# Kernel tuning notes

Hardware: AMD Instinct MI355X
Metric: run time of the kernel (lower is better)

The kernel has to match this reference:

```python
import jax, jax.numpy as jnp
import numpy as np

N = 10000      # nodes
E = 320000     # edges (before self-loops)
D = 256        # d_model
DC = 128       # d_content = d_model // 2
L = 3          # num_layers
K = 4096       # nodes_of_interest
LN_EPS = 1e-5


def setup_inputs() -> dict:
    key = jax.random.key(0)
    ks = jax.random.split(key, 7)
    x = jax.random.normal(ks[0], (N, D), dtype=jnp.float32)
    edge_index = jax.random.randint(ks[1], (2, E), 0, N)
    nodes_of_interest = jax.random.randint(ks[2], (K,), 0, N)
    # per-layer linear weights (stacked over layers)
    Wc = jax.random.normal(ks[3], (L, DC, DC), dtype=jnp.float32) * (1.0 / np.sqrt(DC))
    bc = jnp.zeros((L, DC), dtype=jnp.float32)
    Wp = jax.random.normal(ks[4], (L, DC, DC), dtype=jnp.float32) * (1.0 / np.sqrt(DC))
    bp = jnp.zeros((L, DC), dtype=jnp.float32)
    gamma = jnp.ones((L, D), dtype=jnp.float32)
    beta = jnp.zeros((L, D), dtype=jnp.float32)
    return {"x": x, "edge_index": edge_index, "nodes_of_interest": nodes_of_interest,
            "Wc": Wc, "bc": bc, "Wp": Wp, "bp": bp, "gamma": gamma, "beta": beta}


def _layernorm(h, g, b):
    mu = jnp.mean(h, axis=-1, keepdims=True)
    var = jnp.mean((h - mu) ** 2, axis=-1, keepdims=True)
    return (h - mu) * jax.lax.rsqrt(var + LN_EPS) * g + b


def reference(x, edge_index, nodes_of_interest, Wc, bc, Wp, bp, gamma, beta):
    n = x.shape[0]
    loops = jnp.arange(n)
    # add self-loops (PyG add_self_loops): done per conv in torch but identical each layer
    row = jnp.concatenate([edge_index[0], loops])  # source j
    col = jnp.concatenate([edge_index[1], loops])  # target i
    # symmetric-ish normalization: degree counted over row only (as in source)
    deg = jax.ops.segment_sum(jnp.ones_like(row, dtype=x.dtype), row, num_segments=n)
    dis = deg ** -0.5
    norm = dis[row] * dis[col]  # [E+N]

    def conv(h, l):
        hc = h[:, :DC] @ Wc[l].T + bc[l]
        hp = h[:, DC:] @ Wp[l].T + bp[l]
        ht = jnp.concatenate([hc, hp], axis=-1)
        msg = norm[:, None] * ht[row]                      # gather + normalize
        return jax.ops.segment_sum(msg, col, num_segments=n)  # scatter-add

    for l in range(L - 1):
        x = x + jax.nn.relu(_layernorm(conv(x, l), gamma[l], beta[l]))
    x = x + _layernorm(conv(x, L - 1), gamma[L - 1], beta[L - 1])
    return x[nodes_of_interest]
```

## Files before the change

kernel.cpp:

```cpp
#include <hip/hip_runtime.h>

#define DMODEL 256
#define DCH 128
#define NLAYER 3
#define LN_EPS 1e-5f

__device__ __forceinline__ unsigned short f2bf(float f) {
  unsigned int u = __float_as_uint(f);
  unsigned int r = (u + 0x7FFF + ((u >> 16) & 1)) >> 16;
  return (unsigned short)r;
}


__global__ __launch_bounds__(256) void hist_kernel(const int* __restrict__ row,
    const int* __restrict__ col, int* cnt_row, int* cnt_col, int E) {
  int e = blockIdx.x * 256 + threadIdx.x;
  if (e < E) {
    atomicAdd(&cnt_row[row[e]], 1);
    atomicAdd(&cnt_col[col[e]], 1);
  }
}

__global__ __launch_bounds__(256) void scan_dis_kernel(
    const int* __restrict__ cnt_col, const int* __restrict__ cnt_row,
    int* __restrict__ indptr, int* __restrict__ cursor,
    float* __restrict__ dis, int N, int E) {
  int t = threadIdx.x;
  for (int i = t; i < N; i += 256) dis[i] = rsqrtf((float)(cnt_row[i] + 1));

  const int PER = (N + 255) / 256;
  int start = t * PER;
  int sum = 0;
  for (int k = 0; k < PER; ++k) {
    int i = start + k;
    if (i < N) sum += cnt_col[i];
  }
  int lane = t & 63, wid = t >> 6;
  int inc = sum;
#pragma unroll
  for (int off = 1; off < 64; off <<= 1) {
    int v = __shfl_up(inc, off);
    if (lane >= off) inc += v;
  }
  __shared__ int wsum[4];
  if (lane == 63) wsum[wid] = inc;
  __syncthreads();
  int woff = 0;
  for (int w = 0; w < wid; ++w) woff += wsum[w];
  int run = woff + inc - sum;
  for (int k = 0; k < PER; ++k) {
    int i = start + k;
    if (i < N) {
      indptr[i] = run;
      cursor[i] = run;
      run += cnt_col[i];
    }
  }
  if (t == 255) indptr[N] = E;
}

__global__ __launch_bounds__(256) void fill_kernel(const int* __restrict__ row,
    const int* __restrict__ col, int* cursor, int* __restrict__ idx, int E) {
  int e = blockIdx.x * 256 + threadIdx.x;
  if (e < E) {
    int pos = atomicAdd(&cursor[col[e]], 1);
    idx[pos] = row[e];
  }
}


__global__ __launch_bounds__(256) void gemm_kernel(const float* __restrict__ x,
    const float* __restrict__ Wc, const float* __restrict__ bc,
    const float* __restrict__ Wp, const float* __restrict__ bp,
    unsigned short* __restrict__ ht, int layer, int Nn) {
  int h = blockIdx.y;
  const float* __restrict__ W = (h ? Wp : Wc) + (size_t)layer * DCH * DCH;
  const float* __restrict__ b = (h ? bp : bc) + (size_t)layer * DCH;
  int i0 = blockIdx.x * 32;
  int t = threadIdx.x;
  int tx = t & 31;
  int ty = t >> 5;

  __shared__ float xs[32][128];
  __shared__ float Ws[32][132];

#pragma unroll
  for (int i = 0; i < 4; ++i) {
    int f = t + i * 256;
    int r = f >> 5, cq = f & 31;
    int gi = i0 + r;
    float4 v = make_float4(0.f, 0.f, 0.f, 0.f);
    if (gi < Nn) v = *(const float4*)&x[(size_t)gi * DMODEL + h * DCH + cq * 4];
    *(float4*)&xs[r][cq * 4] = v;
  }

  float acc[4][4];
#pragma unroll
  for (int r = 0; r < 4; ++r)
#pragma unroll
    for (int c = 0; c < 4; ++c) acc[r][c] = 0.f;

  for (int kc = 0; kc < 128; kc += 32) {
    __syncthreads();
#pragma unroll
    for (int i = 0; i < 4; ++i) {
      int f = t + i * 256;
      int o = f >> 3;
      int kq = f & 7;
      float4 v = *(const float4*)&W[o * 128 + kc + kq * 4];
      Ws[kq * 4 + 0][o] = v.x;
      Ws[kq * 4 + 1][o] = v.y;
      Ws[kq * 4 + 2][o] = v.z;
      Ws[kq * 4 + 3][o] = v.w;
    }
    __syncthreads();
#pragma unroll 8
    for (int k = 0; k < 32; ++k) {
      float4 wv = *(const float4*)&Ws[k][tx * 4];
      float xr[4];
#pragma unroll
      for (int r = 0; r < 4; ++r) xr[r] = xs[ty * 4 + r][kc + k];
#pragma unroll
      for (int r = 0; r < 4; ++r) {
        acc[r][0] += xr[r] * wv.x;
        acc[r][1] += xr[r] * wv.y;
        acc[r][2] += xr[r] * wv.z;
        acc[r][3] += xr[r] * wv.w;
      }
    }
  }

  float4 bias = *(const float4*)&b[tx * 4];
#pragma unroll
  for (int r = 0; r < 4; ++r) {
    int gi = i0 + ty * 4 + r;
    if (gi < Nn) {
      ushort4 pk;
      pk.x = f2bf(acc[r][0] + bias.x);
      pk.y = f2bf(acc[r][1] + bias.y);
      pk.z = f2bf(acc[r][2] + bias.z);
      pk.w = f2bf(acc[r][3] + bias.w);
      *(ushort4*)&ht[(size_t)gi * DMODEL + h * DCH + tx * 4] = pk;
    }
  }
}


__global__ __launch_bounds__(128) void agg_kernel(const float* __restrict__ xin,
    const unsigned short* __restrict__ ht, float* __restrict__ xout,
    const float* __restrict__ dis, const int* __restrict__ indptr,
    const int* __restrict__ idx, const float* __restrict__ gamma,
    const float* __restrict__ beta, const int* __restrict__ noi,
    int use_noi, int relu) {
  int b = blockIdx.x;
  int i = use_noi ? noi[b] : b;
  int t = threadIdx.x;
  float di = dis[i];
  size_t rbase = (size_t)i * DMODEL + 2 * t;

  unsigned int us = *(const unsigned int*)&ht[rbase];
  float w2s = di * di;
  float acc0 = w2s * __uint_as_float(us << 16);
  float acc1 = w2s * __uint_as_float(us & 0xFFFF0000u);

  int s = indptr[i], e = indptr[i + 1];
  __shared__ int s_src[128];
  __shared__ float s_w[128];
  for (int base = s; base < e; base += 128) {
    int n = min(128, e - base);
    __syncthreads();
    if (t < n) {
      int sr = idx[base + t];
      s_src[t] = sr;
      s_w[t] = dis[sr] * di;
    }
    __syncthreads();
    for (int j = 0; j < n; ++j) {
      unsigned int u = *(const unsigned int*)&ht[(size_t)s_src[j] * DMODEL + 2 * t];
      float w = s_w[j];
      acc0 += w * __uint_as_float(u << 16);
      acc1 += w * __uint_as_float(u & 0xFFFF0000u);
    }
  }

  float v1 = acc0 + acc1, v2 = acc0 * acc0 + acc1 * acc1;
#pragma unroll
  for (int o = 32; o > 0; o >>= 1) {
    v1 += __shfl_down(v1, o);
    v2 += __shfl_down(v2, o);
  }
  __shared__ float w1[2], w2[2];
  int wid = t >> 6, lane = t & 63;
  if (lane == 0) { w1[wid] = v1; w2[wid] = v2; }
  __syncthreads();
  float s1 = w1[0] + w1[1];
  float s2 = w2[0] + w2[1];
  float mu = s1 * (1.0f / DMODEL);
  float var = s2 * (1.0f / DMODEL) - mu * mu;
  float rs = rsqrtf(var + LN_EPS);
  float2 g = *(const float2*)&gamma[2 * t];
  float2 bb = *(const float2*)&beta[2 * t];
  float y0 = (acc0 - mu) * rs * g.x + bb.x;
  float y1 = (acc1 - mu) * rs * g.y + bb.y;
  if (relu) { y0 = fmaxf(y0, 0.f); y1 = fmaxf(y1, 0.f); }
  float2 xi = *(const float2*)&xin[rbase];
  size_t ob = (size_t)(use_noi ? b : i) * DMODEL + 2 * t;
  *(float2*)&xout[ob] = make_float2(xi.x + y0, xi.y + y1);
}

extern "C" void kernel_launch(void* const* d_in, const int* in_sizes, int n_in,
                              void* d_out, int out_size, void* d_ws, size_t ws_size,
                              hipStream_t stream) {
  const float* x     = (const float*)d_in[0];
  const int*   edges = (const int*)d_in[1];
  const int*   noi   = (const int*)d_in[2];
  const float* Wc    = (const float*)d_in[3];
  const float* bc    = (const float*)d_in[4];
  const float* Wp    = (const float*)d_in[5];
  const float* bp    = (const float*)d_in[6];
  const float* gamma = (const float*)d_in[7];
  const float* beta  = (const float*)d_in[8];

  int N = in_sizes[0] / DMODEL;
  int E = in_sizes[1] / 2;
  int K = in_sizes[2];
  const int* row = edges;
  const int* col = edges + E;

  char* base = (char*)d_ws;
  size_t off = 0;
  auto alloc = [&](size_t bytes) -> void* {
    void* p = base + off;
    off += (bytes + 255) & ~(size_t)255;
    return p;
  };

  float*          xA     = (float*)alloc((size_t)N * DMODEL * 4);
  float*          xB     = (float*)alloc((size_t)N * DMODEL * 4);
  unsigned short* htb    = (unsigned short*)alloc((size_t)N * DMODEL * 2);
  float*          dis    = (float*)alloc((size_t)N * 4);
  int*            cnt    = (int*)alloc((size_t)2 * N * 4);
  int*            indptr = (int*)alloc((size_t)(N + 1) * 4);
  int*            cursor = (int*)alloc((size_t)N * 4);
  int*            idx    = (int*)alloc((size_t)E * 4);

  hipMemsetAsync(cnt, 0, (size_t)2 * N * 4, stream);

  int eb = (E + 255) / 256;
  hist_kernel<<<eb, 256, 0, stream>>>(row, col, cnt, cnt + N, E);
  scan_dis_kernel<<<1, 256, 0, stream>>>(cnt + N, cnt, indptr, cursor, dis, N, E);
  fill_kernel<<<eb, 256, 0, stream>>>(row, col, cursor, idx, E);

  const float* cur_in = x;
  float* bufs[2] = {xA, xB};
  for (int l = 0; l < NLAYER; ++l) {
    dim3 ggrid((N + 31) / 32, 2);
    gemm_kernel<<<ggrid, 256, 0, stream>>>(cur_in, Wc, bc, Wp, bp, htb, l, N);
    if (l < NLAYER - 1) {
      agg_kernel<<<N, 128, 0, stream>>>(cur_in, htb, bufs[l & 1], dis, indptr, idx,
                                        gamma + (size_t)l * DMODEL,
                                        beta + (size_t)l * DMODEL,
                                        nullptr, 0, 1);
      cur_in = bufs[l & 1];
    } else {
      agg_kernel<<<K, 128, 0, stream>>>(cur_in, htb, (float*)d_out, dis, indptr, idx,
                                        gamma + (size_t)l * DMODEL,
                                        beta + (size_t)l * DMODEL,
                                        noi, 1, 0);
    }
  }
}
```

Baseline: 274.4 us.

## Use bf16 MFMA for per-layer linear and unroll edge gather by four

Replaces the FP32 shared-memory tiled GEMM with a bf16 MFMA 16x16x32 kernel that loads x and W rows straight from global memory, converts them to bf16 in registers, and folds the bias into the accumulator init. It also unrolls the aggregation neighbor loop by four so several independent gather loads are in flight at once. Inputs and weights are rounded to bf16 before the multiply, which costs precision. The output stores are scattered 2-byte writes and W is re-read per block without LDS staging.

New measurement: 278.3 us. About the same (+1.4%).

```diff
diff --git a/kernel.cpp b/kernel.cpp
--- a/kernel.cpp
+++ b/kernel.cpp
@@ -1,14 +1,22 @@
 #include <hip/hip_runtime.h>
+#include <hip/hip_bf16.h>
 
 #define DMODEL 256
 #define DCH 128
 #define NLAYER 3
 #define LN_EPS 1e-5f
 
+typedef float f32x4 __attribute__((ext_vector_type(4)));
+typedef short s16x8 __attribute__((ext_vector_type(8)));
+
 __device__ __forceinline__ unsigned short f2bf(float f) {
   unsigned int u = __float_as_uint(f);
   unsigned int r = (u + 0x7FFF + ((u >> 16) & 1)) >> 16;
   return (unsigned short)r;
+}
+
+__device__ __forceinline__ unsigned int pk2bf(float x, float y) {
+  return ((unsigned int)f2bf(y) << 16) | f2bf(x);
 }
 
 
@@ -69,7 +77,7 @@
 }
 
 
-__global__ __launch_bounds__(256) void gemm_kernel(const float* __restrict__ x,
+__global__ __launch_bounds__(256) void gemm_mfma_kernel(const float* __restrict__ x,
     const float* __restrict__ Wc, const float* __restrict__ bc,
     const float* __restrict__ Wp, const float* __restrict__ bp,
     unsigned short* __restrict__ ht, int layer, int Nn) {
@@ -78,73 +86,67 @@
   const float* __restrict__ b = (h ? bp : bc) + (size_t)layer * DCH;
   int i0 = blockIdx.x * 32;
   int t = threadIdx.x;
-  int tx = t & 31;
-  int ty = t >> 5;
-
-  __shared__ float xs[32][128];
-  __shared__ float Ws[32][132];
-
-#pragma unroll
-  for (int i = 0; i < 4; ++i) {
-    int f = t + i * 256;
-    int r = f >> 5, cq = f & 31;
-    int gi = i0 + r;
-    float4 v = make_float4(0.f, 0.f, 0.f, 0.f);
-    if (gi < Nn) v = *(const float4*)&x[(size_t)gi * DMODEL + h * DCH + cq * 4];
-    *(float4*)&xs[r][cq * 4] = v;
-  }
-
-  float acc[4][4];
-#pragma unroll
-  for (int r = 0; r < 4; ++r)
-#pragma unroll
-    for (int c = 0; c < 4; ++c) acc[r][c] = 0.f;
-
-  for (int kc = 0; kc < 128; kc += 32) {
-    __syncthreads();
-#pragma unroll
-    for (int i = 0; i < 4; ++i) {
-      int f = t + i * 256;
-      int o = f >> 3;
-      int kq = f & 7;
-      float4 v = *(const float4*)&W[o * 128 + kc + kq * 4];
-      Ws[kq * 4 + 0][o] = v.x;
-      Ws[kq * 4 + 1][o] = v.y;
-      Ws[kq * 4 + 2][o] = v.z;
-      Ws[kq * 4 + 3][o] = v.w;
-    }
-    __syncthreads();
-#pragma unroll 8
-    for (int k = 0; k < 32; ++k) {
-      float4 wv = *(const float4*)&Ws[k][tx * 4];
-      float xr[4];
-#pragma unroll
-      for (int r = 0; r < 4; ++r) xr[r] = xs[ty * 4 + r][kc + k];
-#pragma unroll
-      for (int r = 0; r < 4; ++r) {
-        acc[r][0] += xr[r] * wv.x;
-        acc[r][1] += xr[r] * wv.y;
-        acc[r][2] += xr[r] * wv.z;
-        acc[r][3] += xr[r] * wv.w;
-      }
-    }
-  }
-
-  float4 bias = *(const float4*)&b[tx * 4];
-#pragma unroll
-  for (int r = 0; r < 4; ++r) {
-    int gi = i0 + ty * 4 + r;
-    if (gi < Nn) {
-      ushort4 pk;
-      pk.x = f2bf(acc[r][0] + bias.x);
-      pk.y = f2bf(acc[r][1] + bias.y);
-      pk.z = f2bf(acc[r][2] + bias.z);
-      pk.w = f2bf(acc[r][3] + bias.w);
-      *(ushort4*)&ht[(size_t)gi * DMODEL + h * DCH + tx * 4] = pk;
-    }
-  }
-}
-
+  int w = t >> 6;
+  int lane = t & 63;
+  int mt = w & 1;
+  int cg = w >> 1;
+  int lrow = lane & 15;
+  int kgrp = lane >> 4;
+
+  int arow = i0 + mt * 16 + lrow;
+  int arow_c = min(arow, Nn - 1);
+  const float* ap = x + (size_t)arow_c * DMODEL + h * DCH + kgrp * 8;
+
+  int bcol[4];
+  const float* bp_[4];
+  f32x4 acc[4];
+#pragma unroll
+  for (int nt = 0; nt < 4; ++nt) {
+    bcol[nt] = cg * 64 + nt * 16 + lrow;
+    bp_[nt] = W + bcol[nt] * DCH + kgrp * 8;
+    float bias = b[bcol[nt]];
+    acc[nt] = (f32x4){bias, bias, bias, bias};
+  }
+
+  union U8 { s16x8 v; unsigned int u[4]; };
+
+#pragma unroll
+  for (int kt = 0; kt < 4; ++kt) {
+    float4 a0 = *(const float4*)(ap + kt * 32);
+    float4 a1 = *(const float4*)(ap + kt * 32 + 4);
+    U8 af;
+    af.u[0] = pk2bf(a0.x, a0.y);
+    af.u[1] = pk2bf(a0.z, a0.w);
+    af.u[2] = pk2bf(a1.x, a1.y);
+    af.u[3] = pk2bf(a1.z, a1.w);
+#pragma unroll
+    for (int nt = 0; nt < 4; ++nt) {
+      float4 b0 = *(const float4*)(bp_[nt] + kt * 32);
+      float4 b1 = *(const float4*)(bp_[nt] + kt * 32 + 4);
+      U8 bf;
+      bf.u[0] = pk2bf(b0.x, b0.y);
+      bf.u[1] = pk2bf(b0.z, b0.w);
+      bf.u[2] = pk2bf(b1.x, b1.y);
+      bf.u[3] = pk2bf(b1.z, b1.w);
+      acc[nt] = __builtin_amdgcn_mfma_f32_16x16x32_bf16(af.v, bf.v, acc[nt], 0, 0, 0);
+    }
+  }
+
+#pragma unroll
+  for (int nt = 0; nt < 4; ++nt) {
+#pragma unroll
+    for (int j = 0; j < 4; ++j) {
+      int gi = i0 + mt * 16 + kgrp * 4 + j;
+      if (gi < Nn) ht[(size_t)gi * DMODEL + h * DCH + bcol[nt]] = f2bf(acc[nt][j]);
+    }
+  }
+}
+
+
+__device__ __forceinline__ void bf2x(unsigned int u, float w, float& a0, float& a1) {
+  a0 += w * __uint_as_float(u << 16);
+  a1 += w * __uint_as_float(u & 0xFFFF0000u);
+}
 
 __global__ __launch_bounds__(128) void agg_kernel(const float* __restrict__ xin,
     const unsigned short* __restrict__ ht, float* __restrict__ xout,
@@ -175,11 +177,22 @@
       s_w[t] = dis[sr] * di;
     }
     __syncthreads();
-    for (int j = 0; j < n; ++j) {
+    int j = 0;
+    for (; j + 4 <= n; j += 4) {
+      int  q0 = s_src[j], q1 = s_src[j + 1], q2 = s_src[j + 2], q3 = s_src[j + 3];
+      float w0 = s_w[j], w1 = s_w[j + 1], w2 = s_w[j + 2], w3 = s_w[j + 3];
+      unsigned int u0 = *(const unsigned int*)&ht[(size_t)q0 * DMODEL + 2 * t];
+      unsigned int u1 = *(const unsigned int*)&ht[(size_t)q1 * DMODEL + 2 * t];
+      unsigned int u2 = *(const unsigned int*)&ht[(size_t)q2 * DMODEL + 2 * t];
+      unsigned int u3 = *(const unsigned int*)&ht[(size_t)q3 * DMODEL + 2 * t];
+      bf2x(u0, w0, acc0, acc1);
+      bf2x(u1, w1, acc0, acc1);
+      bf2x(u2, w2, acc0, acc1);
+      bf2x(u3, w3, acc0, acc1);
+    }
+    for (; j < n; ++j) {
       unsigned int u = *(const unsigned int*)&ht[(size_t)s_src[j] * DMODEL + 2 * t];
-      float w = s_w[j];
-      acc0 += w * __uint_as_float(u << 16);
-      acc1 += w * __uint_as_float(u & 0xFFFF0000u);
+      bf2x(u, s_w[j], acc0, acc1);
     }
   }
 
@@ -189,12 +202,12 @@
     v1 += __shfl_down(v1, o);
     v2 += __shfl_down(v2, o);
   }
-  __shared__ float w1[2], w2[2];
+  __shared__ float w1s[2], w2ss[2];
   int wid = t >> 6, lane = t & 63;
-  if (lane == 0) { w1[wid] = v1; w2[wid] = v2; }
+  if (lane == 0) { w1s[wid] = v1; w2ss[wid] = v2; }
   __syncthreads();
-  float s1 = w1[0] + w1[1];
-  float s2 = w2[0] + w2[1];
+  float s1 = w1s[0] + w1s[1];
+  float s2 = w2ss[0] + w2ss[1];
   float mu = s1 * (1.0f / DMODEL);
   float var = s2 * (1.0f / DMODEL) - mu * mu;
   float rs = rsqrtf(var + LN_EPS);
@@ -255,7 +268,7 @@
   float* bufs[2] = {xA, xB};
   for (int l = 0; l < NLAYER; ++l) {
     dim3 ggrid((N + 31) / 32, 2);
-    gemm_kernel<<<ggrid, 256, 0, stream>>>(cur_in, Wc, bc, Wp, bp, htb, l, N);
+    gemm_mfma_kernel<<<ggrid, 256, 0, stream>>>(cur_in, Wc, bc, Wp, bp, htb, l, N);
     if (l < NLAYER - 1) {
       agg_kernel<<<N, 128, 0, stream>>>(cur_in, htb, bufs[l & 1], dis, indptr, idx,
                                         gamma + (size_t)l * DMODEL,
```
